# Optimization experiments

Measured on AMD Instinct MI355X. Metric: run time of the kernel, lower is better.

The kernel has to match this reference:

```python
import jax, jax.numpy as jnp
import numpy as np

N, E, H, C = 100000, 1600000, 4, 32  # nodes, edges, heads, per-head channels
F_IN, F_HID, F_OUT = 128, 32, 16
NEG_SLOPE = 0.2


def setup_inputs() -> dict:
    key = jax.random.key(0)
    ks = jax.random.split(key, 16)
    s = 0.05
    return {
        "x": jax.random.normal(ks[0], (N, F_IN), jnp.float32),
        "edge_index": jax.random.randint(ks[1], (2, E), 0, N, jnp.int32),
        "W0": jax.random.normal(ks[2], (F_IN, H * C), jnp.float32) * s,
        "att_src0": jax.random.normal(ks[3], (H, C), jnp.float32) * s,
        "att_dst0": jax.random.normal(ks[4], (H, C), jnp.float32) * s,
        "b0": jax.random.normal(ks[5], (H * C,), jnp.float32) * s,
        "W1": jax.random.normal(ks[6], (H * C, H * C), jnp.float32) * s,
        "att_src1": jax.random.normal(ks[7], (H, C), jnp.float32) * s,
        "att_dst1": jax.random.normal(ks[8], (H, C), jnp.float32) * s,
        "b1": jax.random.normal(ks[9], (H * C,), jnp.float32) * s,
        "Wm1": jax.random.normal(ks[10], (H * C, F_HID), jnp.float32) * s,
        "bm1": jax.random.normal(ks[11], (F_HID,), jnp.float32) * s,
        "Wm2": jax.random.normal(ks[12], (F_HID, F_OUT), jnp.float32) * s,
        "bm2": jax.random.normal(ks[13], (F_OUT,), jnp.float32) * s,
    }


def gat_layer(x, src, dst, W, att_src, att_dst, bias):
    n = x.shape[0]
    h = (x @ W).reshape(n, H, C)                       # [N,H,C]
    a_src = jnp.einsum("nhc,hc->nh", h, att_src)       # [N,H]
    a_dst = jnp.einsum("nhc,hc->nh", h, att_dst)       # [N,H]
    e = a_src[src] + a_dst[dst]                        # [E,H]
    e = jnp.where(e > 0, e, NEG_SLOPE * e)             # leaky_relu(0.2)
    m = jax.ops.segment_max(e, dst, num_segments=n)    # [N,H] segment softmax
    ee = jnp.exp(e - m[dst])
    z = jax.ops.segment_sum(ee, dst, num_segments=n)
    alpha = ee / z[dst]                                # [E,H]
    msg = alpha[:, :, None] * h[src]                   # [E,H,C]
    out = jax.ops.segment_sum(msg, dst, num_segments=n)  # [N,H,C]
    return out.reshape(n, H * C) + bias


def reference(x, edge_index, W0, att_src0, att_dst0, b0,
              W1, att_src1, att_dst1, b1, Wm1, bm1, Wm2, bm2):
    src, dst = edge_index[0], edge_index[1]
    x = jax.nn.relu(gat_layer(x, src, dst, W0, att_src0, att_dst0, b0))
    x = jax.nn.relu(gat_layer(x, src, dst, W1, att_src1, att_dst1, b1))
    x = jax.nn.relu(x @ Wm1 + bm1)
    return x @ Wm2 + bm2
```

## Files before the change

kernel.cpp:

```cpp
#include <hip/hip_runtime.h>
#include <hip/hip_bf16.h>

#define NEG 0.2f

typedef __attribute__((ext_vector_type(8))) short short8v;
typedef __attribute__((ext_vector_type(4))) float f32x4;

static __device__ __forceinline__ float bf2f(unsigned int u16){
  return __uint_as_float(u16 << 16);
}
static __device__ __forceinline__ unsigned short f2bf(float f){
  __hip_bfloat16 h = __float2bfloat16(f);
  return *reinterpret_cast<unsigned short*>(&h);
}

#define CHUNK 2048
#define PER_T 8

__global__ __launch_bounds__(256) void k_bcount(
    const int* __restrict__ dst, int* __restrict__ bcnt, int E, int NB)
{
  __shared__ int lc[512];
  int t = threadIdx.x;
  int ebase = blockIdx.x * CHUNK;
  for (int j=t; j<NB; j+=256) lc[j]=0;
  __syncthreads();
  #pragma unroll
  for (int k=0;k<PER_T;++k){
    int i = ebase + t + k*256;
    if (i < E) atomicAdd(&lc[dst[i] >> 8], 1);
  }
  __syncthreads();
  for (int j=t; j<NB; j+=256){
    int c = lc[j];
    if (c) atomicAdd(&bcnt[j], c);
  }
}

__global__ __launch_bounds__(256) void k_bscan(
    const int* __restrict__ bcnt, int* __restrict__ bstart,
    int* __restrict__ bfill, int NB)
{
  __shared__ int sd[256];
  int t = threadIdx.x;
  int i0 = 2*t, i1 = 2*t+1;
  int v0 = (i0<NB) ? bcnt[i0] : 0;
  int v1 = (i1<NB) ? bcnt[i1] : 0;
  int s = v0+v1;
  sd[t]=s; __syncthreads();
  for (int off=1; off<256; off<<=1){
    int x = (t>=off) ? sd[t-off] : 0;
    __syncthreads();
    sd[t] += x;
    __syncthreads();
  }
  int ex = sd[t]-s;
  if (i0<=NB){ bstart[i0]=ex; if(i0<NB) bfill[i0]=ex; }
  ex += v0;
  if (i1<=NB){ bstart[i1]=ex; if(i1<NB) bfill[i1]=ex; }
}

__global__ __launch_bounds__(256) void k_binpass(
    const int* __restrict__ src, const int* __restrict__ dst,
    int* __restrict__ bfill, unsigned int* __restrict__ pairs, int E, int NB)
{
  __shared__ int lcnt[512];
  __shared__ int lbase[512];
  int t = threadIdx.x;
  int ebase = blockIdx.x * CHUNK;
  for (int j=t; j<NB; j+=256) lcnt[j]=0;
  __syncthreads();
  unsigned int pv[PER_T]; int pb[PER_T];
  #pragma unroll
  for (int k=0;k<PER_T;++k){
    int i = ebase + t + k*256;
    pb[k] = -1;
    if (i < E){
      int d = dst[i];
      int s = src[i];
      pb[k] = d >> 8;
      pv[k] = ((unsigned int)s << 8) | (unsigned int)(d & 255);
      atomicAdd(&lcnt[pb[k]], 1);
    }
  }
  __syncthreads();
  for (int j=t; j<NB; j+=256){
    int c = lcnt[j];
    lbase[j] = c ? atomicAdd(&bfill[j], c) : 0;
    lcnt[j] = 0;
  }
  __syncthreads();
  #pragma unroll
  for (int k=0;k<PER_T;++k){
    if (pb[k] >= 0){
      int ofs = atomicAdd(&lcnt[pb[k]], 1);
      pairs[lbase[pb[k]] + ofs] = pv[k];
    }
  }
}

__global__ __launch_bounds__(256) void k_csr(
    const unsigned int* __restrict__ pairs, const int* __restrict__ bstart,
    int* __restrict__ rowptr, int* __restrict__ csr, int n)
{
  __shared__ int lc[256];
  __shared__ int sd[256];
  __shared__ int rp[257];
  int b = blockIdx.x;
  int base = b << 8;
  int t = threadIdx.x;
  int cnt = n - base; if (cnt > 256) cnt = 256;
  int beg = bstart[b], end = bstart[b+1];
  lc[t]=0; __syncthreads();
  for (int i = beg + t; i < end; i += 256)
    atomicAdd(&lc[pairs[i] & 255u], 1);
  __syncthreads();
  int v = lc[t];
  sd[t]=v; __syncthreads();
  for (int off=1; off<256; off<<=1){
    int x = (t>=off) ? sd[t-off] : 0;
    __syncthreads();
    sd[t] += x;
    __syncthreads();
  }
  rp[t+1] = beg + sd[t];
  if (t==0) rp[0] = beg;
  lc[t] = 0;
  __syncthreads();
  if (t < cnt) rowptr[base + t] = rp[t];
  if (t==0 && base + cnt == n) rowptr[n] = rp[cnt];
  for (int i = beg + t; i < end; i += 256){
    unsigned int p = pairs[i];
    int d = (int)(p & 255u);
    int ofs = atomicAdd(&lc[d], 1);
    csr[rp[d] + ofs] = (int)(p >> 8);
  }
}

__global__ void k_wconv(const float* __restrict__ W0, const float* __restrict__ W1,
                        unsigned short* __restrict__ wt0, unsigned short* __restrict__ wt1){
  int b = blockIdx.x;
  const float* W = (b < 64) ? W0 : W1;
  unsigned short* wt = (b < 64) ? wt0 : wt1;
  int i = (b & 63)*256 + threadIdx.x;
  int k = i >> 7, nn = i & 127;
  wt[nn*128 + k] = f2bf(W[i]);
}

template<int IN_BF16>
__global__ __launch_bounds__(256) void k_gemm_att(
    const void* __restrict__ xin_, const unsigned short* __restrict__ wt,
    const float* __restrict__ atts, const float* __restrict__ attd,
    unsigned short* __restrict__ hb, float* __restrict__ as_, float* __restrict__ ad_, int n)
{
  __shared__ __align__(16) unsigned short xls[64*128];
  int t = threadIdx.x;
  int base = blockIdx.x*64;
  int nrem = n - base;
  if (IN_BF16){
    const uint4* Xb = reinterpret_cast<const uint4*>(xin_);
    #pragma unroll
    for (int j=0;j<4;++j){
      int i = t + j*256;
      int row = i >> 4, c16 = i & 15;
      uint4 v = (row < nrem) ? Xb[(size_t)(base+row)*16 + c16]
                             : make_uint4(0,0,0,0);
      int addr = row*256 + ((c16*16) ^ ((row&7)<<4));
      *reinterpret_cast<uint4*>(reinterpret_cast<char*>(xls) + addr) = v;
    }
  } else {
    const float4* X4 = reinterpret_cast<const float4*>(xin_);
    #pragma unroll
    for (int j=0;j<8;++j){
      int i = t + j*256;
      int row = i >> 5, cb = i & 31;
      float4 v = (row < nrem) ? X4[(size_t)(base+row)*32 + cb] : make_float4(0.f,0.f,0.f,0.f);
      unsigned int p0 = (unsigned int)f2bf(v.x) | ((unsigned int)f2bf(v.y)<<16);
      unsigned int p1 = (unsigned int)f2bf(v.z) | ((unsigned int)f2bf(v.w)<<16);
      int addr = row*256 + ((cb*8) ^ ((row&7)<<4));
      *reinterpret_cast<uint2*>(reinterpret_cast<char*>(xls) + addr) = make_uint2(p0,p1);
    }
  }
  __syncthreads();
  int w = t >> 6;
  int l = t & 63;
  int l15 = l & 15, l4 = l >> 4;
  int n0 = w*32;
  short8v bfr[2][4];
  #pragma unroll
  for (int nt=0;nt<2;++nt){
    const unsigned short* bp = wt + (size_t)(n0 + nt*16 + l15)*128 + l4*8;
    #pragma unroll
    for (int kk=0;kk<4;++kk)
      bfr[nt][kk] = *reinterpret_cast<const short8v*>(bp + kk*32);
  }
  f32x4 acc[4][2];
  #pragma unroll
  for (int mt=0;mt<4;++mt)
    #pragma unroll
    for (int nt=0;nt<2;++nt)
      acc[mt][nt] = (f32x4){0.f,0.f,0.f,0.f};
  #pragma unroll
  for (int kk=0;kk<4;++kk){
    short8v afr[4];
    #pragma unroll
    for (int mt=0;mt<4;++mt){
      int row = mt*16 + l15;
      int addr = row*256 + ((kk*64 + l4*16) ^ ((row&7)<<4));
      afr[mt] = *reinterpret_cast<const short8v*>(reinterpret_cast<char*>(xls) + addr);
    }
    #pragma unroll
    for (int mt=0;mt<4;++mt)
      #pragma unroll
      for (int nt=0;nt<2;++nt)
        acc[mt][nt] = __builtin_amdgcn_mfma_f32_16x16x32_bf16(afr[mt], bfr[nt][kk], acc[mt][nt], 0, 0, 0);
  }
  float av0 = atts[n0 + l15],    av1 = atts[n0 + 16 + l15];
  float dv0 = attd[n0 + l15],    dv1 = attd[n0 + 16 + l15];
  #pragma unroll
  for (int mt=0;mt<4;++mt){
    #pragma unroll
    for (int r=0;r<4;++r){
      float ps = acc[mt][0][r]*av0 + acc[mt][1][r]*av1;
      float pd = acc[mt][0][r]*dv0 + acc[mt][1][r]*dv1;
      ps += __shfl_xor(ps,1); ps += __shfl_xor(ps,2);
      ps += __shfl_xor(ps,4); ps += __shfl_xor(ps,8);
      pd += __shfl_xor(pd,1); pd += __shfl_xor(pd,2);
      pd += __shfl_xor(pd,4); pd += __shfl_xor(pd,8);
      int node = base + mt*16 + l4*4 + r;
      if (l15==0 && node < n){
        as_[node*4 + w] = ps;
        ad_[node*4 + w] = pd;
      }
    }
  }
  __syncthreads();
  #pragma unroll
  for (int mt=0;mt<4;++mt)
    #pragma unroll
    for (int nt=0;nt<2;++nt)
      #pragma unroll
      for (int r=0;r<4;++r){
        int row = mt*16 + l4*4 + r;
        int col = n0 + nt*16 + l15;
        xls[row*128 + col] = f2bf(acc[mt][nt][r]);
      }
  __syncthreads();
  const uint4* xsrc = reinterpret_cast<const uint4*>(xls);
  uint4* hdst = reinterpret_cast<uint4*>(hb + (size_t)base*128);
  #pragma unroll
  for (int j=0;j<4;++j){
    int i = t + j*256;
    int row = i >> 4;
    if (row < nrem) hdst[i] = xsrc[i];
  }
}

__global__ __launch_bounds__(256) void k_aggr(
    const unsigned short* __restrict__ hb, const float* __restrict__ as_,
    const float* __restrict__ ad_, const int* __restrict__ rowptr,
    const int* __restrict__ csr, const float* __restrict__ bias,
    unsigned short* __restrict__ out, int n)
{
  int wid = (int)((blockIdx.x*(size_t)blockDim.x + threadIdx.x) >> 6);
  int lane = threadIdx.x & 63;
  if (wid >= n) return;
  int half = lane >> 5;
  int li   = lane & 31;
  int c0   = li*4;
  int head = li >> 3;
  float adn = ad_[wid*4 + head];
  int beg = rowptr[wid], end = rowptr[wid+1];
  int deg = end - beg;
  float4 acc = make_float4(0.f,0.f,0.f,0.f);
  float z = 0.f;
  int nfull = deg & ~7;
  int lim = beg + nfull;
  int i = beg + half*4;
  int s0=0,s1=0,s2=0,s3=0;
  if (i < lim){ s0=csr[i]; s1=csr[i+1]; s2=csr[i+2]; s3=csr[i+3]; }
  for (; i < lim; ){
    int ni = i + 8;
    int t0=0,t1=0,t2=0,t3=0;
    if (ni < lim){ t0=csr[ni]; t1=csr[ni+1]; t2=csr[ni+2]; t3=csr[ni+3]; }
    float e0 = as_[s0*4+head];
    float e1 = as_[s1*4+head];
    float e2 = as_[s2*4+head];
    float e3 = as_[s3*4+head];
    uint2 p0 = *reinterpret_cast<const uint2*>(hb + (size_t)s0*128 + c0);
    uint2 p1 = *reinterpret_cast<const uint2*>(hb + (size_t)s1*128 + c0);
    uint2 p2 = *reinterpret_cast<const uint2*>(hb + (size_t)s2*128 + c0);
    uint2 p3 = *reinterpret_cast<const uint2*>(hb + (size_t)s3*128 + c0);
    e0 += adn; e1 += adn; e2 += adn; e3 += adn;
    e0 = (e0>0.f)?e0:NEG*e0;
    e1 = (e1>0.f)?e1:NEG*e1;
    e2 = (e2>0.f)?e2:NEG*e2;
    e3 = (e3>0.f)?e3:NEG*e3;
    float x0 = __expf(e0);
    float x1 = __expf(e1);
    float x2 = __expf(e2);
    float x3 = __expf(e3);
    z += (x0+x1)+(x2+x3);
    acc.x = fmaf(x0, bf2f(p0.x & 0xffffu), acc.x);
    acc.y = fmaf(x0, bf2f(p0.x >> 16),     acc.y);
    acc.z = fmaf(x0, bf2f(p0.y & 0xffffu), acc.z);
    acc.w = fmaf(x0, bf2f(p0.y >> 16),     acc.w);
    acc.x = fmaf(x1, bf2f(p1.x & 0xffffu), acc.x);
    acc.y = fmaf(x1, bf2f(p1.x >> 16),     acc.y);
    acc.z = fmaf(x1, bf2f(p1.y & 0xffffu), acc.z);
    acc.w = fmaf(x1, bf2f(p1.y >> 16),     acc.w);
    acc.x = fmaf(x2, bf2f(p2.x & 0xffffu), acc.x);
    acc.y = fmaf(x2, bf2f(p2.x >> 16),     acc.y);
    acc.z = fmaf(x2, bf2f(p2.y & 0xffffu), acc.z);
    acc.w = fmaf(x2, bf2f(p2.y >> 16),     acc.w);
    acc.x = fmaf(x3, bf2f(p3.x & 0xffffu), acc.x);
    acc.y = fmaf(x3, bf2f(p3.x >> 16),     acc.y);
    acc.z = fmaf(x3, bf2f(p3.y & 0xffffu), acc.z);
    acc.w = fmaf(x3, bf2f(p3.y >> 16),     acc.w);
    i = ni; s0=t0; s1=t1; s2=t2; s3=t3;
  }
  for (int j = beg + nfull + half; j < end; j += 2){
    int s = csr[j];
    float e = as_[s*4+head] + adn;
    e = (e>0.f)?e:NEG*e;
    float ee = __expf(e);
    z += ee;
    uint2 pv = *reinterpret_cast<const uint2*>(hb + (size_t)s*128 + c0);
    acc.x = fmaf(ee, bf2f(pv.x & 0xffffu), acc.x);
    acc.y = fmaf(ee, bf2f(pv.x >> 16),     acc.y);
    acc.z = fmaf(ee, bf2f(pv.y & 0xffffu), acc.z);
    acc.w = fmaf(ee, bf2f(pv.y >> 16),     acc.w);
  }
  z     += __shfl_xor(z, 32);
  acc.x += __shfl_xor(acc.x, 32);
  acc.y += __shfl_xor(acc.y, 32);
  acc.z += __shfl_xor(acc.z, 32);
  acc.w += __shfl_xor(acc.w, 32);
  if (half == 0){
    float4 o;
    if (deg > 0){
      float rz = 1.f/z;
      o.x = fmaxf(fmaf(acc.x,rz,bias[c0  ]), 0.f);
      o.y = fmaxf(fmaf(acc.y,rz,bias[c0+1]), 0.f);
      o.z = fmaxf(fmaf(acc.z,rz,bias[c0+2]), 0.f);
      o.w = fmaxf(fmaf(acc.w,rz,bias[c0+3]), 0.f);
    } else {
      o.x = fmaxf(bias[c0  ], 0.f);
      o.y = fmaxf(bias[c0+1], 0.f);
      o.z = fmaxf(bias[c0+2], 0.f);
      o.w = fmaxf(bias[c0+3], 0.f);
    }
    unsigned int lo = (unsigned int)f2bf(o.x) | ((unsigned int)f2bf(o.y)<<16);
    unsigned int hi = (unsigned int)f2bf(o.z) | ((unsigned int)f2bf(o.w)<<16);
    *reinterpret_cast<uint2*>(out + (size_t)wid*128 + c0) = make_uint2(lo,hi);
  }
}

__global__ __launch_bounds__(256) void k_mlp(
    const unsigned short* __restrict__ xb, const float* __restrict__ Wm1, const float* __restrict__ bm1,
    const float* __restrict__ Wm2, const float* __restrict__ bm2,
    float* __restrict__ out, int n)
{
  __shared__ float xs[64*129];
  __shared__ float w1s[128*32];
  __shared__ float hs[64*33];
  __shared__ float w2s[32*16];
  __shared__ float b1s[32];
  __shared__ float b2s[16];
  int t = threadIdx.x;
  int base = blockIdx.x*64;
  const uint4* Xb = reinterpret_cast<const uint4*>(xb);
  #pragma unroll
  for (int j=0;j<4;++j){
    int i = t + j*256;
    int row = i >> 4, seg = i & 15;
    uint4 v = (base+row < n) ? Xb[(size_t)(base+row)*16 + seg] : make_uint4(0,0,0,0);
    float* xp = &xs[row*129 + seg*8];
    xp[0] = bf2f(v.x & 0xffffu); xp[1] = bf2f(v.x >> 16);
    xp[2] = bf2f(v.y & 0xffffu); xp[3] = bf2f(v.y >> 16);
    xp[4] = bf2f(v.z & 0xffffu); xp[5] = bf2f(v.z >> 16);
    xp[6] = bf2f(v.w & 0xffffu); xp[7] = bf2f(v.w >> 16);
  }
  for (int i=t; i<128*32; i+=256) w1s[i]=Wm1[i];
  for (int i=t; i<32*16;  i+=256) w2s[i]=Wm2[i];
  if (t<32) b1s[t]=bm1[t];
  if (t<16) b2s[t]=bm2[t];
  __syncthreads();
  int l = t&63, g = t>>6;
  float hid[8];
  #pragma unroll
  for (int j=0;j<8;++j) hid[j]=0.f;
  for (int k=0;k<128;++k){
    float xk = xs[l*129+k];
    #pragma unroll
    for (int j=0;j<8;++j) hid[j] = fmaf(xk, w1s[k*32 + g*8 + j], hid[j]);
  }
  #pragma unroll
  for (int j=0;j<8;++j) hs[l*33 + g*8 + j] = fmaxf(hid[j] + b1s[g*8+j], 0.f);
  __syncthreads();
  float o[4] = {0.f,0.f,0.f,0.f};
  for (int k=0;k<32;++k){
    float xv = hs[l*33+k];
    #pragma unroll
    for (int j=0;j<4;++j) o[j] = fmaf(xv, w2s[k*16 + g*4 + j], o[j]);
  }
  int node = base + l;
  if (node < n){
    #pragma unroll
    for (int j=0;j<4;++j) out[(size_t)node*16 + g*4 + j] = o[j] + b2s[g*4+j];
  }
}

extern "C" void kernel_launch(void* const* d_in, const int* in_sizes, int n_in,
                              void* d_out, int out_size, void* d_ws, size_t ws_size,
                              hipStream_t stream)
{
  const float* x   = (const float*)d_in[0];
  const int*   ei  = (const int*)  d_in[1];
  const float* W0  = (const float*)d_in[2];
  const float* as0 = (const float*)d_in[3];
  const float* ad0 = (const float*)d_in[4];
  const float* b0  = (const float*)d_in[5];
  const float* W1  = (const float*)d_in[6];
  const float* as1 = (const float*)d_in[7];
  const float* ad1 = (const float*)d_in[8];
  const float* b1  = (const float*)d_in[9];
  const float* Wm1 = (const float*)d_in[10];
  const float* bm1 = (const float*)d_in[11];
  const float* Wm2 = (const float*)d_in[12];
  const float* bm2 = (const float*)d_in[13];
  int N = in_sizes[0]/128;
  int E = in_sizes[1]/2;
  const int* srcI = ei;
  const int* dstI = ei + E;

  char* ws = (char*)d_ws;
  size_t off = 0;
  auto alloc = [&](size_t bytes)->void*{
    void* p = ws + off; off += (bytes + 255) & ~(size_t)255; return p;
  };
  unsigned short* hbuf = (unsigned short*)alloc((size_t)N*128*2);
  unsigned short* xbuf = (unsigned short*)alloc((size_t)N*128*2);
  float* asb   = (float*)alloc((size_t)N*4*4);
  float* adb   = (float*)alloc((size_t)N*4*4);
  int* rowptr  = (int*)alloc((size_t)(N+1)*4);
  int* bcnt    = (int*)alloc(2048);
  int* bstart  = (int*)alloc(2052);
  int* bfill   = (int*)alloc(2048);
  int* csr     = (int*)alloc((size_t)E*4);
  unsigned int* pairs = (unsigned int*)alloc((size_t)E*4);
  unsigned short* wt0 = (unsigned short*)alloc(128*128*2);
  unsigned short* wt1 = (unsigned short*)alloc(128*128*2);
  (void)ws_size; (void)n_in; (void)out_size;

  int NB = (N + 255) >> 8;
  int gC = (E + CHUNK - 1) / CHUNK;
  hipMemsetAsync(bcnt, 0, 2048, stream);
  k_bcount <<<gC,256,0,stream>>>(dstI, bcnt, E, NB);
  k_bscan  <<<1, 256,0,stream>>>(bcnt, bstart, bfill, NB);
  k_binpass<<<gC,256,0,stream>>>(srcI, dstI, bfill, pairs, E, NB);
  k_csr    <<<NB,256,0,stream>>>(pairs, bstart, rowptr, csr, N);
  k_wconv  <<<128,256,0,stream>>>(W0, W1, wt0, wt1);

  int gG = (N+63)/64;
  int gA = (int)(((size_t)N*64 + 255)/256);
  k_gemm_att<0><<<gG,256,0,stream>>>(x,    wt0, as0, ad0, hbuf, asb, adb, N);
  k_aggr       <<<gA,256,0,stream>>>(hbuf, asb, adb, rowptr, csr, b0, xbuf, N);
  k_gemm_att<1><<<gG,256,0,stream>>>(xbuf, wt1, as1, ad1, hbuf, asb, adb, N);
  k_aggr       <<<gA,256,0,stream>>>(hbuf, asb, adb, rowptr, csr, b1, xbuf, N);
  k_mlp        <<<gG,256,0,stream>>>(xbuf, Wm1, bm1, Wm2, bm2, (float*)d_out, N);
}
```

Before: 302.7 us.

## Merge independent kernels via block-index dispatch to overlap graph build with GEMM

Weight conversion is folded into the edge-count kernel, and the first-layer GEMM+attention is folded into the edge binning pass, each using a block-index split to choose the work. This cuts kernel launches and lets the CSR construction run concurrently with the dense projection instead of serially. In exchange the merged kernel's shared memory is the sum of both parts' allocations, which may lower occupancy, and the block scheduling mixes heterogeneous workloads.

```diff
diff --git a/kernel.cpp b/kernel.cpp
--- a/kernel.cpp
+++ b/kernel.cpp
@@ -17,12 +17,13 @@
 #define CHUNK 2048
 #define PER_T 8
 
-__global__ __launch_bounds__(256) void k_bcount(
-    const int* __restrict__ dst, int* __restrict__ bcnt, int E, int NB)
-{
-  __shared__ int lc[512];
+
+static __device__ __forceinline__ void bcount_body(
+    const int* __restrict__ dst, int* __restrict__ bcnt, int E, int NB,
+    int blk, int* lc)
+{
   int t = threadIdx.x;
-  int ebase = blockIdx.x * CHUNK;
+  int ebase = blk * CHUNK;
   for (int j=t; j<NB; j+=256) lc[j]=0;
   __syncthreads();
   #pragma unroll
@@ -34,6 +35,172 @@
   for (int j=t; j<NB; j+=256){
     int c = lc[j];
     if (c) atomicAdd(&bcnt[j], c);
+  }
+}
+
+static __device__ __forceinline__ void binpass_body(
+    const int* __restrict__ src, const int* __restrict__ dst,
+    int* __restrict__ bfill, unsigned int* __restrict__ pairs, int E, int NB,
+    int blk, int* lcnt, int* lbase)
+{
+  int t = threadIdx.x;
+  int ebase = blk * CHUNK;
+  for (int j=t; j<NB; j+=256) lcnt[j]=0;
+  __syncthreads();
+  unsigned int pv[PER_T]; int pb[PER_T];
+  #pragma unroll
+  for (int k=0;k<PER_T;++k){
+    int i = ebase + t + k*256;
+    pb[k] = -1;
+    if (i < E){
+      int d = dst[i];
+      int s = src[i];
+      pb[k] = d >> 8;
+      pv[k] = ((unsigned int)s << 8) | (unsigned int)(d & 255);
+      atomicAdd(&lcnt[pb[k]], 1);
+    }
+  }
+  __syncthreads();
+  for (int j=t; j<NB; j+=256){
+    int c = lcnt[j];
+    lbase[j] = c ? atomicAdd(&bfill[j], c) : 0;
+    lcnt[j] = 0;
+  }
+  __syncthreads();
+  #pragma unroll
+  for (int k=0;k<PER_T;++k){
+    if (pb[k] >= 0){
+      int ofs = atomicAdd(&lcnt[pb[k]], 1);
+      pairs[lbase[pb[k]] + ofs] = pv[k];
+    }
+  }
+}
+
+template<int IN_BF16>
+static __device__ __forceinline__ void gemm_att_body(
+    const void* __restrict__ xin_, const unsigned short* __restrict__ wt,
+    const float* __restrict__ atts, const float* __restrict__ attd,
+    unsigned short* __restrict__ hb, float* __restrict__ as_, float* __restrict__ ad_,
+    int n, int blk, unsigned short* xls)
+{
+  int t = threadIdx.x;
+  int base = blk*64;
+  int nrem = n - base;
+  if (IN_BF16){
+    const uint4* Xb = reinterpret_cast<const uint4*>(xin_);
+    #pragma unroll
+    for (int j=0;j<4;++j){
+      int i = t + j*256;
+      int row = i >> 4, c16 = i & 15;
+      uint4 v = (row < nrem) ? Xb[(size_t)(base+row)*16 + c16]
+                             : make_uint4(0,0,0,0);
+      int addr = row*256 + ((c16*16) ^ ((row&7)<<4));
+      *reinterpret_cast<uint4*>(reinterpret_cast<char*>(xls) + addr) = v;
+    }
+  } else {
+    const float4* X4 = reinterpret_cast<const float4*>(xin_);
+    #pragma unroll
+    for (int j=0;j<8;++j){
+      int i = t + j*256;
+      int row = i >> 5, cb = i & 31;
+      float4 v = (row < nrem) ? X4[(size_t)(base+row)*32 + cb] : make_float4(0.f,0.f,0.f,0.f);
+      unsigned int p0 = (unsigned int)f2bf(v.x) | ((unsigned int)f2bf(v.y)<<16);
+      unsigned int p1 = (unsigned int)f2bf(v.z) | ((unsigned int)f2bf(v.w)<<16);
+      int addr = row*256 + ((cb*8) ^ ((row&7)<<4));
+      *reinterpret_cast<uint2*>(reinterpret_cast<char*>(xls) + addr) = make_uint2(p0,p1);
+    }
+  }
+  __syncthreads();
+  int w = t >> 6;
+  int l = t & 63;
+  int l15 = l & 15, l4 = l >> 4;
+  int n0 = w*32;
+  short8v bfr[2][4];
+  #pragma unroll
+  for (int nt=0;nt<2;++nt){
+    const unsigned short* bp = wt + (size_t)(n0 + nt*16 + l15)*128 + l4*8;
+    #pragma unroll
+    for (int kk=0;kk<4;++kk)
+      bfr[nt][kk] = *reinterpret_cast<const short8v*>(bp + kk*32);
+  }
+  f32x4 acc[4][2];
+  #pragma unroll
+  for (int mt=0;mt<4;++mt)
+    #pragma unroll
+    for (int nt=0;nt<2;++nt)
+      acc[mt][nt] = (f32x4){0.f,0.f,0.f,0.f};
+  #pragma unroll
+  for (int kk=0;kk<4;++kk){
+    short8v afr[4];
+    #pragma unroll
+    for (int mt=0;mt<4;++mt){
+      int row = mt*16 + l15;
+      int addr = row*256 + ((kk*64 + l4*16) ^ ((row&7)<<4));
+      afr[mt] = *reinterpret_cast<const short8v*>(reinterpret_cast<char*>(xls) + addr);
+    }
+    #pragma unroll
+    for (int mt=0;mt<4;++mt)
+      #pragma unroll
+      for (int nt=0;nt<2;++nt)
+        acc[mt][nt] = __builtin_amdgcn_mfma_f32_16x16x32_bf16(afr[mt], bfr[nt][kk], acc[mt][nt], 0, 0, 0);
+  }
+  float av0 = atts[n0 + l15],    av1 = atts[n0 + 16 + l15];
+  float dv0 = attd[n0 + l15],    dv1 = attd[n0 + 16 + l15];
+  #pragma unroll
+  for (int mt=0;mt<4;++mt){
+    #pragma unroll
+    for (int r=0;r<4;++r){
+      float ps = acc[mt][0][r]*av0 + acc[mt][1][r]*av1;
+      float pd = acc[mt][0][r]*dv0 + acc[mt][1][r]*dv1;
+      ps += __shfl_xor(ps,1); ps += __shfl_xor(ps,2);
+      ps += __shfl_xor(ps,4); ps += __shfl_xor(ps,8);
+      pd += __shfl_xor(pd,1); pd += __shfl_xor(pd,2);
+      pd += __shfl_xor(pd,4); pd += __shfl_xor(pd,8);
+      int node = base + mt*16 + l4*4 + r;
+      if (l15==0 && node < n){
+        as_[node*4 + w] = ps;
+        ad_[node*4 + w] = pd;
+      }
+    }
+  }
+  __syncthreads();
+  #pragma unroll
+  for (int mt=0;mt<4;++mt)
+    #pragma unroll
+    for (int nt=0;nt<2;++nt)
+      #pragma unroll
+      for (int r=0;r<4;++r){
+        int row = mt*16 + l4*4 + r;
+        int col = n0 + nt*16 + l15;
+        xls[row*128 + col] = f2bf(acc[mt][nt][r]);
+      }
+  __syncthreads();
+  const uint4* xsrc = reinterpret_cast<const uint4*>(xls);
+  uint4* hdst = reinterpret_cast<uint4*>(hb + (size_t)base*128);
+  #pragma unroll
+  for (int j=0;j<4;++j){
+    int i = t + j*256;
+    int row = i >> 4;
+    if (row < nrem) hdst[i] = xsrc[i];
+  }
+}
+
+
+__global__ __launch_bounds__(256) void k_wconv_bcount(
+    const float* __restrict__ W0, const float* __restrict__ W1,
+    unsigned short* __restrict__ wt0, unsigned short* __restrict__ wt1,
+    const int* __restrict__ dst, int* __restrict__ bcnt, int E, int NB)
+{
+  __shared__ int lc[512];
+  int b = blockIdx.x;
+  if (b < 128){
+    const float* W = (b < 64) ? W0 : W1;
+    unsigned short* wt = (b < 64) ? wt0 : wt1;
+    int i = (b & 63)*256 + threadIdx.x;
+    int k = i >> 7, nn = i & 127;
+    wt[nn*128 + k] = f2bf(W[i]);
+  } else {
+    bcount_body(dst, bcnt, E, NB, b - 128, lc);
   }
 }
 
@@ -60,43 +227,32 @@
   if (i1<=NB){ bstart[i1]=ex; if(i1<NB) bfill[i1]=ex; }
 }
 
-__global__ __launch_bounds__(256) void k_binpass(
+__global__ __launch_bounds__(256) void k_gemm1_binpass(
+    const float* __restrict__ xin, const unsigned short* __restrict__ wt,
+    const float* __restrict__ atts, const float* __restrict__ attd,
+    unsigned short* __restrict__ hb, float* __restrict__ as_, float* __restrict__ ad_,
+    int n, int nG,
     const int* __restrict__ src, const int* __restrict__ dst,
     int* __restrict__ bfill, unsigned int* __restrict__ pairs, int E, int NB)
 {
+  __shared__ __align__(16) unsigned short xls[64*128];
   __shared__ int lcnt[512];
   __shared__ int lbase[512];
-  int t = threadIdx.x;
-  int ebase = blockIdx.x * CHUNK;
-  for (int j=t; j<NB; j+=256) lcnt[j]=0;
-  __syncthreads();
-  unsigned int pv[PER_T]; int pb[PER_T];
-  #pragma unroll
-  for (int k=0;k<PER_T;++k){
-    int i = ebase + t + k*256;
-    pb[k] = -1;
-    if (i < E){
-      int d = dst[i];
-      int s = src[i];
-      pb[k] = d >> 8;
-      pv[k] = ((unsigned int)s << 8) | (unsigned int)(d & 255);
-      atomicAdd(&lcnt[pb[k]], 1);
-    }
-  }
-  __syncthreads();
-  for (int j=t; j<NB; j+=256){
-    int c = lcnt[j];
-    lbase[j] = c ? atomicAdd(&bfill[j], c) : 0;
-    lcnt[j] = 0;
-  }
-  __syncthreads();
-  #pragma unroll
-  for (int k=0;k<PER_T;++k){
-    if (pb[k] >= 0){
-      int ofs = atomicAdd(&lcnt[pb[k]], 1);
-      pairs[lbase[pb[k]] + ofs] = pv[k];
-    }
-  }
+  int b = blockIdx.x;
+  if (b < nG){
+    gemm_att_body<0>(xin, wt, atts, attd, hb, as_, ad_, n, b, xls);
+  } else {
+    binpass_body(src, dst, bfill, pairs, E, NB, b - nG, lcnt, lbase);
+  }
+}
+
+__global__ __launch_bounds__(256) void k_gemm2(
+    const unsigned short* __restrict__ xin, const unsigned short* __restrict__ wt,
+    const float* __restrict__ atts, const float* __restrict__ attd,
+    unsigned short* __restrict__ hb, float* __restrict__ as_, float* __restrict__ ad_, int n)
+{
+  __shared__ __align__(16) unsigned short xls[64*128];
+  gemm_att_body<1>(xin, wt, atts, attd, hb, as_, ad_, n, blockIdx.x, xls);
 }
 
 __global__ __launch_bounds__(256) void k_csr(
@@ -134,125 +290,6 @@
     int d = (int)(p & 255u);
     int ofs = atomicAdd(&lc[d], 1);
     csr[rp[d] + ofs] = (int)(p >> 8);
-  }
-}
-
-__global__ void k_wconv(const float* __restrict__ W0, const float* __restrict__ W1,
-                        unsigned short* __restrict__ wt0, unsigned short* __restrict__ wt1){
-  int b = blockIdx.x;
-  const float* W = (b < 64) ? W0 : W1;
-  unsigned short* wt = (b < 64) ? wt0 : wt1;
-  int i = (b & 63)*256 + threadIdx.x;
-  int k = i >> 7, nn = i & 127;
-  wt[nn*128 + k] = f2bf(W[i]);
-}
-
-template<int IN_BF16>
-__global__ __launch_bounds__(256) void k_gemm_att(
-    const void* __restrict__ xin_, const unsigned short* __restrict__ wt,
-    const float* __restrict__ atts, const float* __restrict__ attd,
-    unsigned short* __restrict__ hb, float* __restrict__ as_, float* __restrict__ ad_, int n)
-{
-  __shared__ __align__(16) unsigned short xls[64*128];
-  int t = threadIdx.x;
-  int base = blockIdx.x*64;
-  int nrem = n - base;
-  if (IN_BF16){
-    const uint4* Xb = reinterpret_cast<const uint4*>(xin_);
-    #pragma unroll
-    for (int j=0;j<4;++j){
-      int i = t + j*256;
-      int row = i >> 4, c16 = i & 15;
-      uint4 v = (row < nrem) ? Xb[(size_t)(base+row)*16 + c16]
-                             : make_uint4(0,0,0,0);
-      int addr = row*256 + ((c16*16) ^ ((row&7)<<4));
-      *reinterpret_cast<uint4*>(reinterpret_cast<char*>(xls) + addr) = v;
-    }
-  } else {
-    const float4* X4 = reinterpret_cast<const float4*>(xin_);
-    #pragma unroll
-    for (int j=0;j<8;++j){
-      int i = t + j*256;
-      int row = i >> 5, cb = i & 31;
-      float4 v = (row < nrem) ? X4[(size_t)(base+row)*32 + cb] : make_float4(0.f,0.f,0.f,0.f);
-      unsigned int p0 = (unsigned int)f2bf(v.x) | ((unsigned int)f2bf(v.y)<<16);
-      unsigned int p1 = (unsigned int)f2bf(v.z) | ((unsigned int)f2bf(v.w)<<16);
-      int addr = row*256 + ((cb*8) ^ ((row&7)<<4));
-      *reinterpret_cast<uint2*>(reinterpret_cast<char*>(xls) + addr) = make_uint2(p0,p1);
-    }
-  }
-  __syncthreads();
-  int w = t >> 6;
-  int l = t & 63;
-  int l15 = l & 15, l4 = l >> 4;
-  int n0 = w*32;
-  short8v bfr[2][4];
-  #pragma unroll
-  for (int nt=0;nt<2;++nt){
-    const unsigned short* bp = wt + (size_t)(n0 + nt*16 + l15)*128 + l4*8;
-    #pragma unroll
-    for (int kk=0;kk<4;++kk)
-      bfr[nt][kk] = *reinterpret_cast<const short8v*>(bp + kk*32);
-  }
-  f32x4 acc[4][2];
-  #pragma unroll
-  for (int mt=0;mt<4;++mt)
-    #pragma unroll
-    for (int nt=0;nt<2;++nt)
-      acc[mt][nt] = (f32x4){0.f,0.f,0.f,0.f};
-  #pragma unroll
-  for (int kk=0;kk<4;++kk){
-    short8v afr[4];
-    #pragma unroll
-    for (int mt=0;mt<4;++mt){
-      int row = mt*16 + l15;
-      int addr = row*256 + ((kk*64 + l4*16) ^ ((row&7)<<4));
-      afr[mt] = *reinterpret_cast<const short8v*>(reinterpret_cast<char*>(xls) + addr);
-    }
-    #pragma unroll
-    for (int mt=0;mt<4;++mt)
-      #pragma unroll
-      for (int nt=0;nt<2;++nt)
-        acc[mt][nt] = __builtin_amdgcn_mfma_f32_16x16x32_bf16(afr[mt], bfr[nt][kk], acc[mt][nt], 0, 0, 0);
-  }
-  float av0 = atts[n0 + l15],    av1 = atts[n0 + 16 + l15];
-  float dv0 = attd[n0 + l15],    dv1 = attd[n0 + 16 + l15];
-  #pragma unroll
-  for (int mt=0;mt<4;++mt){
-    #pragma unroll
-    for (int r=0;r<4;++r){
-      float ps = acc[mt][0][r]*av0 + acc[mt][1][r]*av1;
-      float pd = acc[mt][0][r]*dv0 + acc[mt][1][r]*dv1;
-      ps += __shfl_xor(ps,1); ps += __shfl_xor(ps,2);
-      ps += __shfl_xor(ps,4); ps += __shfl_xor(ps,8);
-      pd += __shfl_xor(pd,1); pd += __shfl_xor(pd,2);
-      pd += __shfl_xor(pd,4); pd += __shfl_xor(pd,8);
-      int node = base + mt*16 + l4*4 + r;
-      if (l15==0 && node < n){
-        as_[node*4 + w] = ps;
-        ad_[node*4 + w] = pd;
-      }
-    }
-  }
-  __syncthreads();
-  #pragma unroll
-  for (int mt=0;mt<4;++mt)
-    #pragma unroll
-    for (int nt=0;nt<2;++nt)
-      #pragma unroll
-      for (int r=0;r<4;++r){
-        int row = mt*16 + l4*4 + r;
-        int col = n0 + nt*16 + l15;
-        xls[row*128 + col] = f2bf(acc[mt][nt][r]);
-      }
-  __syncthreads();
-  const uint4* xsrc = reinterpret_cast<const uint4*>(xls);
-  uint4* hdst = reinterpret_cast<uint4*>(hb + (size_t)base*128);
-  #pragma unroll
-  for (int j=0;j<4;++j){
-    int i = t + j*256;
-    int row = i >> 4;
-    if (row < nrem) hdst[i] = xsrc[i];
   }
 }
 
@@ -455,18 +492,17 @@
 
   int NB = (N + 255) >> 8;
   int gC = (E + CHUNK - 1) / CHUNK;
-  hipMemsetAsync(bcnt, 0, 2048, stream);
-  k_bcount <<<gC,256,0,stream>>>(dstI, bcnt, E, NB);
-  k_bscan  <<<1, 256,0,stream>>>(bcnt, bstart, bfill, NB);
-  k_binpass<<<gC,256,0,stream>>>(srcI, dstI, bfill, pairs, E, NB);
-  k_csr    <<<NB,256,0,stream>>>(pairs, bstart, rowptr, csr, N);
-  k_wconv  <<<128,256,0,stream>>>(W0, W1, wt0, wt1);
-
   int gG = (N+63)/64;
   int gA = (int)(((size_t)N*64 + 255)/256);
-  k_gemm_att<0><<<gG,256,0,stream>>>(x,    wt0, as0, ad0, hbuf, asb, adb, N);
-  k_aggr       <<<gA,256,0,stream>>>(hbuf, asb, adb, rowptr, csr, b0, xbuf, N);
-  k_gemm_att<1><<<gG,256,0,stream>>>(xbuf, wt1, as1, ad1, hbuf, asb, adb, N);
-  k_aggr       <<<gA,256,0,stream>>>(hbuf, asb, adb, rowptr, csr, b1, xbuf, N);
-  k_mlp        <<<gG,256,0,stream>>>(xbuf, Wm1, bm1, Wm2, bm2, (float*)d_out, N);
-}
+
+  hipMemsetAsync(bcnt, 0, 2048, stream);
+  k_wconv_bcount<<<128+gC,256,0,stream>>>(W0, W1, wt0, wt1, dstI, bcnt, E, NB);
+  k_bscan       <<<1,256,0,stream>>>(bcnt, bstart, bfill, NB);
+  k_gemm1_binpass<<<gG+gC,256,0,stream>>>(x, wt0, as0, ad0, hbuf, asb, adb, N, gG,
+                                          srcI, dstI, bfill, pairs, E, NB);
+  k_csr         <<<NB,256,0,stream>>>(pairs, bstart, rowptr, csr, N);
+  k_aggr        <<<gA,256,0,stream>>>(hbuf, asb, adb, rowptr, csr, b0, xbuf, N);
+  k_gemm2       <<<gG,256,0,stream>>>(xbuf, wt1, as1, ad1, hbuf, asb, adb, N);
+  k_aggr        <<<gA,256,0,stream>>>(hbuf, asb, adb, rowptr, csr, b1, xbuf, N);
+  k_mlp         <<<gG,256,0,stream>>>(xbuf, Wm1, bm1, Wm2, bm2, (float*)d_out, N);
+}
```

Result: faster. 286.9 us (-5.2%).
